# Kernel optimization log

Hardware: AMD Instinct MI355X
Metric: run time of the kernel (lower is better)

Reference implementation:

```python
import jax, jax.numpy as jnp
import numpy as np

ROT = 256  # Hadamard block size (ConvLinear4bit._n)


def _hadamard(n):
    # Sylvester construction of the n x n Hadamard matrix (n power of 2)
    H = np.array([[1.0]], dtype=np.float32)
    while H.shape[0] < n:
        H = np.block([[H, H], [H, -H]])
    return jnp.asarray(H / np.sqrt(n), dtype=jnp.float32)


def setup_inputs() -> dict:
    key = jax.random.key(0)
    k1, k2, k3, k4 = jax.random.split(key, 4)
    N, D_in, D_out = 4096, 4096, 4096
    x = jax.random.normal(k1, (N, D_in), dtype=jnp.float32)
    # unpacked int4 weights in [-7, 7] (logical content of the packed uint8 buffer)
    weight_int = jax.random.randint(k2, (D_out, D_in), -7, 8, dtype=jnp.int32)
    # per-output-row weight scales (quarot: max|W_rot| / 7)
    w_scale = jax.random.uniform(k3, (D_out, 1), dtype=jnp.float32) * 0.01 + 1e-4
    bias = jax.random.normal(k4, (D_out,), dtype=jnp.float32) * 0.01
    return {"x": x, "weight_int": weight_int, "w_scale": w_scale, "bias": bias}


def reference(x, weight_int, w_scale, bias):
    N, D = x.shape
    H = _hadamard(ROT)
    # blockwise Hadamard rotation along the feature dim (D is a multiple of ROT)
    x_rot = (x.reshape(N, D // ROT, ROT) @ H).reshape(N, D)
    # per-row symmetric int4 quantization of activations
    scales_x = jnp.max(jnp.abs(x_rot), axis=-1, keepdims=True) / 7.0  # [N, 1]
    q_x = jnp.clip(jnp.round(x_rot / scales_x), -8, 7).astype(jnp.int32)
    acc = jnp.matmul(q_x, weight_int.T)
    # sym_dequant: row scale (activations) * col scale (weights), then bias
    out = acc.astype(jnp.float32) * scales_x * w_scale.T + bias
    return out
```

## Files before the change

kernel.cpp:

```cpp
#include <hip/hip_runtime.h>
#include <math.h>

typedef int v4i  __attribute__((ext_vector_type(4)));
typedef int v16i __attribute__((ext_vector_type(16)));

#define DIM 4096
#define BT 128
#define KT 128
#define TILE (BT * KT)

__device__ __forceinline__ void async16(const void* g, void* l) {
    __builtin_amdgcn_global_load_lds((__attribute__((address_space(1))) void*)(g),
                                     (__attribute__((address_space(3))) void*)(l),
                                     16, 0, 0);
}

#define VMCNT(N) asm volatile("s_waitcnt vmcnt(" #N ")" ::: "memory")
#define BARRIER() asm volatile("s_barrier" ::: "memory")

__global__ __launch_bounds__(256) void prep(const float* __restrict__ x,
                                            const int* __restrict__ w,
                                            signed char* __restrict__ q,
                                            signed char* __restrict__ w8,
                                            float* __restrict__ scales) {
    if (blockIdx.x >= 4096) {
        int i = (blockIdx.x - 4096) * 256 + threadIdx.x;
        int4 v = ((const int4*)w)[i];
        char4 c;
        c.x = (signed char)v.x; c.y = (signed char)v.y;
        c.z = (signed char)v.z; c.w = (signed char)v.w;
        ((char4*)w8)[i] = c;
        return;
    }
    const int row  = blockIdx.x;
    const int lane = threadIdx.x & 63;
    const int wave = threadIdx.x >> 6;
    const float4* xr4 = (const float4*)(x + (size_t)row * DIM);

    float sgn[6];
    #pragma unroll
    for (int i = 0; i < 6; ++i) sgn[i] = (lane & (1 << i)) ? -1.0f : 1.0f;

    float f[4][4];
    #pragma unroll
    for (int b = 0; b < 4; ++b) {
        const int blk = wave + 4 * b;
        float4 v = xr4[blk * 64 + lane];
        float t0 = v.x + v.y, t1 = v.x - v.y;
        float t2 = v.z + v.w, t3 = v.z - v.w;
        f[b][0] = t0 + t2; f[b][1] = t1 + t3;
        f[b][2] = t0 - t2; f[b][3] = t1 - t3;
        #pragma unroll
        for (int st = 0; st < 6; ++st) {
            const int m = 1 << st;
            #pragma unroll
            for (int j = 0; j < 4; ++j) {
                float p = __shfl_xor(f[b][j], m, 64);
                f[b][j] = fmaf(sgn[st], f[b][j], p);
            }
        }
        #pragma unroll
        for (int j = 0; j < 4; ++j) f[b][j] *= 0.0625f;
    }

    float m = 0.0f;
    #pragma unroll
    for (int b = 0; b < 4; ++b)
        #pragma unroll
        for (int j = 0; j < 4; ++j) m = fmaxf(m, fabsf(f[b][j]));
    #pragma unroll
    for (int d = 32; d; d >>= 1) m = fmaxf(m, __shfl_xor(m, d, 64));
    __shared__ float sm[4];
    if (lane == 0) sm[wave] = m;
    __syncthreads();
    m = fmaxf(fmaxf(sm[0], sm[1]), fmaxf(sm[2], sm[3]));

    const float s = m / 7.0f;
    if (threadIdx.x == 0) scales[row] = s;

    char4* qr4 = (char4*)(q + (size_t)row * DIM);
    #pragma unroll
    for (int b = 0; b < 4; ++b) {
        const int blk = wave + 4 * b;
        char4 c;
        int qi;
        qi = (int)rintf(f[b][0] / s); c.x = (signed char)min(7, max(-8, qi));
        qi = (int)rintf(f[b][1] / s); c.y = (signed char)min(7, max(-8, qi));
        qi = (int)rintf(f[b][2] / s); c.z = (signed char)min(7, max(-8, qi));
        qi = (int)rintf(f[b][3] / s); c.w = (signed char)min(7, max(-8, qi));
        qr4[blk * 64 + lane] = c;
    }
}

__global__ __launch_bounds__(256) void gemm_q8(const signed char* __restrict__ A,
                                               const signed char* __restrict__ B,
                                               const float* __restrict__ rowScale,
                                               const float* __restrict__ wscale,
                                               const float* __restrict__ bias,
                                               float* __restrict__ out) {
    __shared__ __align__(16) signed char S[4 * TILE];

    const int flat = blockIdx.y * gridDim.x + blockIdx.x;
    const int xcd  = flat & 7;
    const int idx  = flat >> 3;
    const int bm   = ((xcd >> 1) << 3) + (idx & 7);
    const int bn   = ((xcd & 1) << 4) + (idx >> 3);

    const int t = threadIdx.x;
    const int lane = t & 63, wave = t >> 6;
    const int wm = (wave >> 1) * 64, wn = (wave & 1) * 64;
    const int l31 = lane & 31, lh = lane >> 5;

    const signed char* ga[4];
    const signed char* gb[4];
    #pragma unroll
    for (int h = 0; h < 4; ++h) {
        const int cidx = t + 256 * h;
        const int row  = cidx >> 3;
        const int g    = (cidx & 7) ^ (row & 7);
        ga[h] = A + (size_t)(bm * BT + row) * DIM + g * 16;
        gb[h] = B + (size_t)(bn * BT + row) * DIM + g * 16;
    }

    int offA[2][4], offB[2][4];
    #pragma unroll
    for (int i = 0; i < 2; ++i)
        #pragma unroll
        for (int s = 0; s < 4; ++s) {
            const int r  = wm + i * 32 + l31;
            const int c  = wn + i * 32 + l31;
            const int cl = 2 * s + lh;
            offA[i][s] = r * KT + ((cl ^ (r & 7)) * 16);
            offB[i][s] = c * KT + ((cl ^ (c & 7)) * 16) + TILE;
        }

    v16i acc[2][2] = {};

#define STAGE(P) do {                                                          \
        _Pragma("unroll")                                                      \
        for (int h = 0; h < 4; ++h) {                                          \
            const int l = (P) * 2 * TILE + (t + 256 * h) * 16;                 \
            async16(ga[h], &S[l]);        ga[h] += KT;                         \
            async16(gb[h], &S[l + TILE]); gb[h] += KT;                         \
        }                                                                      \
    } while (0)

#define COMPUTE(P) do {                                                        \
        __builtin_amdgcn_s_setprio(1);                                         \
        _Pragma("unroll")                                                      \
        for (int s = 0; s < 4; ++s) {                                          \
            const v4i a0 = *(const v4i*)&S[(P) * 2 * TILE + offA[0][s]];       \
            const v4i a1 = *(const v4i*)&S[(P) * 2 * TILE + offA[1][s]];       \
            const v4i b0 = *(const v4i*)&S[(P) * 2 * TILE + offB[0][s]];       \
            const v4i b1 = *(const v4i*)&S[(P) * 2 * TILE + offB[1][s]];       \
            acc[0][0] = __builtin_amdgcn_mfma_i32_32x32x32_i8(a0, b0, acc[0][0], 0, 0, 0); \
            acc[0][1] = __builtin_amdgcn_mfma_i32_32x32x32_i8(a0, b1, acc[0][1], 0, 0, 0); \
            acc[1][0] = __builtin_amdgcn_mfma_i32_32x32x32_i8(a1, b0, acc[1][0], 0, 0, 0); \
            acc[1][1] = __builtin_amdgcn_mfma_i32_32x32x32_i8(a1, b1, acc[1][1], 0, 0, 0); \
        }                                                                      \
        __builtin_amdgcn_s_setprio(0);                                         \
    } while (0)

    STAGE(0);
    #pragma unroll 1
    for (int it = 0; it < 15; ++it) {
        STAGE(1); VMCNT(8); BARRIER();
        COMPUTE(0);
        BARRIER();
        STAGE(0); VMCNT(8); BARRIER();
        COMPUTE(1);
        BARRIER();
    }
    STAGE(1); VMCNT(8); BARRIER();
    COMPUTE(0);
    BARRIER();
    VMCNT(0); BARRIER();
    COMPUTE(1);

#undef STAGE
#undef COMPUTE

    #pragma unroll
    for (int j = 0; j < 2; ++j) {
        const int col = bn * BT + wn + j * 32 + l31;
        const float ws = wscale[col];
        const float bs = bias[col];
        #pragma unroll
        for (int i = 0; i < 2; ++i) {
            const int rb = bm * BT + wm + i * 32 + 4 * lh;
            #pragma unroll
            for (int r = 0; r < 16; ++r) {
                const int row = rb + (r & 3) + 8 * (r >> 2);
                out[(size_t)row * DIM + col] =
                    ((float)acc[i][j][r] * rowScale[row]) * ws + bs;
            }
        }
    }
}

extern "C" void kernel_launch(void* const* d_in, const int* in_sizes, int n_in,
                              void* d_out, int out_size, void* d_ws, size_t ws_size,
                              hipStream_t stream) {
    const float* x      = (const float*)d_in[0];
    const int*   wint   = (const int*)d_in[1];
    const float* wscale = (const float*)d_in[2];
    const float* bias   = (const float*)d_in[3];
    float* out = (float*)d_out;

    signed char* q8 = (signed char*)d_ws;
    signed char* w8 = q8 + (size_t)DIM * DIM;
    float* sx = (float*)(w8 + (size_t)DIM * DIM);

    prep<<<4096 + 16384, 256, 0, stream>>>(x, wint, q8, w8, sx);
    gemm_q8<<<dim3(DIM / BT, DIM / BT), 256, 0, stream>>>(q8, w8, sx, wscale, bias, out);
}
```

Measured before the change: 240.5 us.

## Enlarge GEMM tiles to 256x256 with 512 threads and 4-stage LDS pipeline

Changes the int8 MFMA GEMM from 128x128x128 tiles with 256 threads and double buffering to 256x256x64 tiles with 512 threads (8 waves, each computing 128x64) and a four-deep async global-to-LDS pipeline. A new XOR swizzle fits the 64-byte K rows. Larger output tiles double the MFMA work per LDS fragment read and halve global re-reads of A and B. Deeper prefetch hides load latency. In exchange, 128 KB of LDS per block limits each CU to one block, and the grid shrinks to 256 blocks, which risks load imbalance and lower latency hiding.

```diff
diff --git a/kernel.cpp b/kernel.cpp
--- a/kernel.cpp
+++ b/kernel.cpp
@@ -5,9 +5,10 @@
 typedef int v16i __attribute__((ext_vector_type(16)));
 
 #define DIM 4096
-#define BT 128
-#define KT 128
-#define TILE (BT * KT)
+#define BM 256
+#define BK 64
+#define ATILE (BM * BK)
+#define BUFSZ (2 * ATILE)
 
 __device__ __forceinline__ void async16(const void* g, void* l) {
     __builtin_amdgcn_global_load_lds((__attribute__((address_space(1))) void*)(g),
@@ -17,6 +18,10 @@
 
 #define VMCNT(N) asm volatile("s_waitcnt vmcnt(" #N ")" ::: "memory")
 #define BARRIER() asm volatile("s_barrier" ::: "memory")
+
+__device__ __forceinline__ int swzC(int r) {
+    return ((r >> 1) & 3) ^ ((r >> 3) & 3);
+}
 
 __global__ __launch_bounds__(256) void prep(const float* __restrict__ x,
                                             const int* __restrict__ w,
@@ -92,102 +97,112 @@
     }
 }
 
-__global__ __launch_bounds__(256) void gemm_q8(const signed char* __restrict__ A,
-                                               const signed char* __restrict__ B,
-                                               const float* __restrict__ rowScale,
-                                               const float* __restrict__ wscale,
-                                               const float* __restrict__ bias,
-                                               float* __restrict__ out) {
-    __shared__ __align__(16) signed char S[4 * TILE];
+__global__ __launch_bounds__(512, 2) void gemm_q8(const signed char* __restrict__ A,
+                                                  const signed char* __restrict__ B,
+                                                  const float* __restrict__ rowScale,
+                                                  const float* __restrict__ wscale,
+                                                  const float* __restrict__ bias,
+                                                  float* __restrict__ out) {
+    __shared__ __align__(16) signed char S[4 * BUFSZ];
 
     const int flat = blockIdx.y * gridDim.x + blockIdx.x;
     const int xcd  = flat & 7;
     const int idx  = flat >> 3;
-    const int bm   = ((xcd >> 1) << 3) + (idx & 7);
-    const int bn   = ((xcd & 1) << 4) + (idx >> 3);
+    const int bm   = ((xcd >> 1) << 2) + (idx & 3);
+    const int bn   = ((xcd & 1) << 3) + (idx >> 2);
 
     const int t = threadIdx.x;
-    const int lane = t & 63, wave = t >> 6;
-    const int wm = (wave >> 1) * 64, wn = (wave & 1) * 64;
+    const int lane = t & 63;
+    const int wave = t >> 6;
+    const int wm = (wave >> 2) * 128;
+    const int wn = (wave & 3) * 64;
     const int l31 = lane & 31, lh = lane >> 5;
 
-    const signed char* ga[4];
-    const signed char* gb[4];
-    #pragma unroll
-    for (int h = 0; h < 4; ++h) {
-        const int cidx = t + 256 * h;
-        const int row  = cidx >> 3;
-        const int g    = (cidx & 7) ^ (row & 7);
-        ga[h] = A + (size_t)(bm * BT + row) * DIM + g * 16;
-        gb[h] = B + (size_t)(bn * BT + row) * DIM + g * 16;
-    }
-
-    int offA[2][4], offB[2][4];
-    #pragma unroll
-    for (int i = 0; i < 2; ++i)
-        #pragma unroll
-        for (int s = 0; s < 4; ++s) {
-            const int r  = wm + i * 32 + l31;
-            const int c  = wn + i * 32 + l31;
-            const int cl = 2 * s + lh;
-            offA[i][s] = r * KT + ((cl ^ (r & 7)) * 16);
-            offB[i][s] = c * KT + ((cl ^ (c & 7)) * 16) + TILE;
-        }
-
-    v16i acc[2][2] = {};
+    const signed char* ga[2];
+    const signed char* gb[2];
+    int ldsA[2], ldsB[2];
+    #pragma unroll
+    for (int h = 0; h < 2; ++h) {
+        const int cidx = t + 512 * h;
+        const int row  = cidx >> 2;
+        const int g    = (cidx & 3) ^ swzC(row);
+        ga[h] = A + (size_t)(bm * BM + row) * DIM + g * 16;
+        gb[h] = B + (size_t)(bn * BM + row) * DIM + g * 16;
+        ldsA[h] = cidx * 16;
+        ldsB[h] = ATILE + cidx * 16;
+    }
+
+    int offA[4][2], offB[2][2];
+    #pragma unroll
+    for (int i = 0; i < 4; ++i)
+        #pragma unroll
+        for (int s = 0; s < 2; ++s) {
+            const int r = wm + i * 32 + l31;
+            offA[i][s] = r * BK + (((2 * s + lh) ^ swzC(r)) * 16);
+        }
+    #pragma unroll
+    for (int j = 0; j < 2; ++j)
+        #pragma unroll
+        for (int s = 0; s < 2; ++s) {
+            const int c = wn + j * 32 + l31;
+            offB[j][s] = ATILE + c * BK + (((2 * s + lh) ^ swzC(c)) * 16);
+        }
+
+    v16i acc[4][2] = {};
 
 #define STAGE(P) do {                                                          \
-        _Pragma("unroll")                                                      \
-        for (int h = 0; h < 4; ++h) {                                          \
-            const int l = (P) * 2 * TILE + (t + 256 * h) * 16;                 \
-            async16(ga[h], &S[l]);        ga[h] += KT;                         \
-            async16(gb[h], &S[l + TILE]); gb[h] += KT;                         \
-        }                                                                      \
+        async16(ga[0], &S[(P) * BUFSZ + ldsA[0]]); ga[0] += BK;                \
+        async16(ga[1], &S[(P) * BUFSZ + ldsA[1]]); ga[1] += BK;                \
+        async16(gb[0], &S[(P) * BUFSZ + ldsB[0]]); gb[0] += BK;                \
+        async16(gb[1], &S[(P) * BUFSZ + ldsB[1]]); gb[1] += BK;                \
     } while (0)
 
 #define COMPUTE(P) do {                                                        \
         __builtin_amdgcn_s_setprio(1);                                         \
         _Pragma("unroll")                                                      \
-        for (int s = 0; s < 4; ++s) {                                          \
-            const v4i a0 = *(const v4i*)&S[(P) * 2 * TILE + offA[0][s]];       \
-            const v4i a1 = *(const v4i*)&S[(P) * 2 * TILE + offA[1][s]];       \
-            const v4i b0 = *(const v4i*)&S[(P) * 2 * TILE + offB[0][s]];       \
-            const v4i b1 = *(const v4i*)&S[(P) * 2 * TILE + offB[1][s]];       \
+        for (int s = 0; s < 2; ++s) {                                          \
+            const v4i a0 = *(const v4i*)&S[(P) * BUFSZ + offA[0][s]];          \
+            const v4i a1 = *(const v4i*)&S[(P) * BUFSZ + offA[1][s]];          \
+            const v4i a2 = *(const v4i*)&S[(P) * BUFSZ + offA[2][s]];          \
+            const v4i a3 = *(const v4i*)&S[(P) * BUFSZ + offA[3][s]];          \
+            const v4i b0 = *(const v4i*)&S[(P) * BUFSZ + offB[0][s]];          \
+            const v4i b1 = *(const v4i*)&S[(P) * BUFSZ + offB[1][s]];          \
             acc[0][0] = __builtin_amdgcn_mfma_i32_32x32x32_i8(a0, b0, acc[0][0], 0, 0, 0); \
             acc[0][1] = __builtin_amdgcn_mfma_i32_32x32x32_i8(a0, b1, acc[0][1], 0, 0, 0); \
             acc[1][0] = __builtin_amdgcn_mfma_i32_32x32x32_i8(a1, b0, acc[1][0], 0, 0, 0); \
             acc[1][1] = __builtin_amdgcn_mfma_i32_32x32x32_i8(a1, b1, acc[1][1], 0, 0, 0); \
+            acc[2][0] = __builtin_amdgcn_mfma_i32_32x32x32_i8(a2, b0, acc[2][0], 0, 0, 0); \
+            acc[2][1] = __builtin_amdgcn_mfma_i32_32x32x32_i8(a2, b1, acc[2][1], 0, 0, 0); \
+            acc[3][0] = __builtin_amdgcn_mfma_i32_32x32x32_i8(a3, b0, acc[3][0], 0, 0, 0); \
+            acc[3][1] = __builtin_amdgcn_mfma_i32_32x32x32_i8(a3, b1, acc[3][1], 0, 0, 0); \
         }                                                                      \
         __builtin_amdgcn_s_setprio(0);                                         \
     } while (0)
 
-    STAGE(0);
+    STAGE(0); STAGE(1); STAGE(2);
     #pragma unroll 1
     for (int it = 0; it < 15; ++it) {
-        STAGE(1); VMCNT(8); BARRIER();
-        COMPUTE(0);
-        BARRIER();
-        STAGE(0); VMCNT(8); BARRIER();
-        COMPUTE(1);
-        BARRIER();
-    }
-    STAGE(1); VMCNT(8); BARRIER();
-    COMPUTE(0);
-    BARRIER();
-    VMCNT(0); BARRIER();
-    COMPUTE(1);
+        VMCNT(8); BARRIER(); STAGE(3); COMPUTE(0);
+        VMCNT(8); BARRIER(); STAGE(0); COMPUTE(1);
+        VMCNT(8); BARRIER(); STAGE(1); COMPUTE(2);
+        VMCNT(8); BARRIER(); STAGE(2); COMPUTE(3);
+    }
+    VMCNT(8); BARRIER(); STAGE(3); COMPUTE(0);
+    VMCNT(8); BARRIER();           COMPUTE(1);
+    VMCNT(4); BARRIER();           COMPUTE(2);
+    VMCNT(0); BARRIER();           COMPUTE(3);
 
 #undef STAGE
 #undef COMPUTE
 
     #pragma unroll
     for (int j = 0; j < 2; ++j) {
-        const int col = bn * BT + wn + j * 32 + l31;
+        const int col = bn * BM + wn + j * 32 + l31;
         const float ws = wscale[col];
         const float bs = bias[col];
         #pragma unroll
-        for (int i = 0; i < 2; ++i) {
-            const int rb = bm * BT + wm + i * 32 + 4 * lh;
+        for (int i = 0; i < 4; ++i) {
+            const int rb = bm * BM + wm + i * 32 + 4 * lh;
             #pragma unroll
             for (int r = 0; r < 16; ++r) {
                 const int row = rb + (r & 3) + 8 * (r >> 2);
@@ -212,5 +227,5 @@
     float* sx = (float*)(w8 + (size_t)DIM * DIM);
 
     prep<<<4096 + 16384, 256, 0, stream>>>(x, wint, q8, w8, sx);
-    gemm_q8<<<dim3(DIM / BT, DIM / BT), 256, 0, stream>>>(q8, w8, sx, wscale, bias, out);
-}
+    gemm_q8<<<dim3(DIM / BM, DIM / BM), 512, 0, stream>>>(q8, w8, sx, wscale, bias, out);
+}
```

Result: no change. 243.5 us (+1.3%).
